# Performance work log

Hardware: AMD Instinct MI355X
Metric: run time of the kernel (lower is better)

Reference implementation:

```python
import jax, jax.numpy as jnp
import numpy as np

EMBED_DIM = 1024
N_HEADS = 16
HEAD_DIM = EMBED_DIM // N_HEADS
CHUNK = 64  # reward_data_gen_params['chunk_size']
B, T = 8, 1024


def setup_inputs() -> dict:
    key = jax.random.key(0)
    ks = jax.random.split(key, 9)
    s = 0.02
    return {
        "x": jax.random.normal(ks[0], (B, T, EMBED_DIM), dtype=jnp.float32),
        "Wq": jax.random.normal(ks[1], (EMBED_DIM, EMBED_DIM), dtype=jnp.float32) * s,
        "bq": jax.random.normal(ks[2], (EMBED_DIM,), dtype=jnp.float32) * s,
        "Wk": jax.random.normal(ks[3], (EMBED_DIM, EMBED_DIM), dtype=jnp.float32) * s,
        "bk": jax.random.normal(ks[4], (EMBED_DIM,), dtype=jnp.float32) * s,
        "Wv": jax.random.normal(ks[5], (EMBED_DIM, EMBED_DIM), dtype=jnp.float32) * s,
        "bv": jax.random.normal(ks[6], (EMBED_DIM,), dtype=jnp.float32) * s,
        "Wo": jax.random.normal(ks[7], (EMBED_DIM, EMBED_DIM), dtype=jnp.float32) * s,
        "bo": jax.random.normal(ks[8], (EMBED_DIM,), dtype=jnp.float32) * s,
        "attn_scale": jnp.full((1,), 1.0 / np.sqrt(HEAD_DIM), dtype=jnp.float32),
    }


def reference(x, Wq, bq, Wk, bk, Wv, bv, Wo, bo, attn_scale):
    Bsz, Tlen, C = x.shape
    H, D = N_HEADS, HEAD_DIM
    # torch Linear: y = x @ W.T + b
    q = (x @ Wq.T + bq).reshape(Bsz, Tlen, H, D).transpose(0, 2, 1, 3)  # [B,H,T,D]
    k = (x @ Wk.T + bk).reshape(Bsz, Tlen, H, D).transpose(0, 2, 1, 3)
    v = (x @ Wv.T + bv).reshape(Bsz, Tlen, H, D).transpose(0, 2, 1, 3)

    scores = jnp.einsum("bhqd,bhkd->bhqk", q, k) * attn_scale[0]  # [B,H,T,T]

    # Faithful reproduction of the chunked masking: the source only masks when
    # query-chunk >= key-chunk, which (given key>query implies key-chunk>=query-chunk)
    # reduces to masking key>query ONLY inside diagonal CHUNK x CHUNK blocks.
    idx = jnp.arange(Tlen)
    same_block = (idx[:, None] // CHUNK) == (idx[None, :] // CHUNK)
    mask = (idx[None, :] > idx[:, None]) & same_block  # [T,T] True => masked
    scores = jnp.where(mask[None, None], -jnp.inf, scores)

    w = jax.nn.softmax(scores, axis=-1)
    out = jnp.einsum("bhqk,bhkd->bhqd", w, v)  # [B,H,T,D]
    out = out.transpose(0, 2, 1, 3).reshape(Bsz, Tlen, C)
    return out @ Wo.T + bo
```

## Files before the change

### kernel.cpp

```cpp
#include <hip/hip_runtime.h>


typedef __bf16 bf16;
typedef __bf16 bf16x4 __attribute__((ext_vector_type(4)));
typedef __bf16 bf16x8 __attribute__((ext_vector_type(8)));
typedef float  f32x4  __attribute__((ext_vector_type(4)));

#define LOG2E 1.44269504088896340736f

__device__ __forceinline__ void async16(const bf16* g, bf16* l) {
  __builtin_amdgcn_global_load_lds(
      (const __attribute__((address_space(1))) void*)g,
      (__attribute__((address_space(3))) void*)l, 16, 0, 0);
}

#if __has_builtin(__builtin_amdgcn_exp2f)
#define EXP2F(x) __builtin_amdgcn_exp2f(x)
#else
#define EXP2F(x) exp2f(x)
#endif

__global__ __launch_bounds__(256) void k_convert(
    const float* __restrict__ x, const float* __restrict__ wq,
    const float* __restrict__ wk, const float* __restrict__ wv,
    const float* __restrict__ wo, bf16* __restrict__ xb, bf16* __restrict__ wb) {
  const int XV = (8192 * 1024) / 4;
  const int WV = (1024 * 1024) / 4;
  int i = blockIdx.x * 256 + threadIdx.x;
  const float4* src;
  bf16* dst;
  if (i < XV) {
    src = (const float4*)x + i;
    dst = xb + (size_t)i * 4;
  } else {
    int j = i - XV;
    int w = j >> 18;
    int r = j & (WV - 1);
    const float* s = (w == 0) ? wq : (w == 1) ? wk : (w == 2) ? wv : wo;
    src = (const float4*)s + r;
    dst = wb + (size_t)w * (1024 * 1024) + (size_t)r * 4;
  }
  float4 f = *src;
  bf16 tmp[4] = {(bf16)f.x, (bf16)f.y, (bf16)f.z, (bf16)f.w};
  *(uint2*)dst = *(uint2*)tmp;
}

__global__ __launch_bounds__(256) void k_gemm_qkv(
    const bf16* __restrict__ A, const bf16* __restrict__ W,
    const float* __restrict__ bq, const float* __restrict__ bk,
    const float* __restrict__ bv, const float* __restrict__ scale_p,
    bf16* __restrict__ qb, bf16* __restrict__ kb, bf16* __restrict__ vb) {
  __shared__ __attribute__((aligned(16))) bf16 As[8192];
  __shared__ __attribute__((aligned(16))) bf16 Bs[8192];
  const int tid = threadIdx.x, lane = tid & 63, wid = tid >> 6;
  const int quad = lane >> 4, l16 = lane & 15;
  const int wm = (wid & 1) * 64, wn = (wid >> 1) * 64;
  const int tileM = blockIdx.x * 128, tileN = blockIdx.y * 128;

  const int krow = lane >> 3;
  const int gc = (lane & 7) ^ krow;
  const bf16* Ap = A + (size_t)(tileM + wid * 8 + krow) * 1024 + gc * 8;
  const bf16* Bp = W + (size_t)(tileN + wid * 8 + krow) * 1024 + gc * 8;
  const int wofs = wid * 512;
  const int s7 = l16 & 7;

  f32x4 acc[4][4];
#pragma unroll
  for (int i = 0; i < 4; i++)
#pragma unroll
    for (int j = 0; j < 4; j++) acc[i][j] = (f32x4){0.f, 0.f, 0.f, 0.f};

  for (int it = 0; it < 16; it++) {
    const int k0 = it * 64;
#pragma unroll
    for (int rd = 0; rd < 4; rd++) {
      async16(Ap + (size_t)rd * 32768 + k0, &As[rd * 2048 + wofs]);
      async16(Bp + (size_t)rd * 32768 + k0, &Bs[rd * 2048 + wofs]);
    }
    __syncthreads();
#pragma unroll
    for (int kh = 0; kh < 2; kh++) {
      const int pc = ((kh * 4 + quad) ^ s7) * 8;
      bf16x8 af[4], bfr[4];
#pragma unroll
      for (int i = 0; i < 4; i++)
        af[i] = *(const bf16x8*)&As[(wm + i * 16 + l16) * 64 + pc];
#pragma unroll
      for (int j = 0; j < 4; j++)
        bfr[j] = *(const bf16x8*)&Bs[(wn + j * 16 + l16) * 64 + pc];
#pragma unroll
      for (int i = 0; i < 4; i++)
#pragma unroll
        for (int j = 0; j < 4; j++)
          acc[i][j] = __builtin_amdgcn_mfma_f32_16x16x32_bf16(af[i], bfr[j], acc[i][j], 0, 0, 0);
    }
    __syncthreads();
  }

  float qscale = scale_p[0] * LOG2E;
#pragma unroll
  for (int i = 0; i < 4; i++) {
    int m0 = tileM + wm + i * 16 + quad * 4;
    int b = m0 >> 10;
    int t0 = m0 & 1023;
#pragma unroll
    for (int j = 0; j < 4; j++) {
      int n = tileN + wn + j * 16 + l16;
      int which = n >> 10;
      int nm = n & 1023;
      int h = nm >> 6, d = nm & 63;
      float bias = ((which == 0) ? bq : (which == 1) ? bk : bv)[nm];
      if (which == 2) {
        bf16 tmp[4];
#pragma unroll
        for (int r = 0; r < 4; r++) tmp[r] = (bf16)(acc[i][j][r] + bias);
        size_t vidx = (((size_t)((b * 16 + h) * 64 + d)) << 10) | (size_t)t0;
        *(uint2*)&vb[vidx] = *(uint2*)tmp;
      } else {
#pragma unroll
        for (int r = 0; r < 4; r++) {
          float v = acc[i][j][r] + bias;
          size_t idx = (((size_t)(b * 16 + h) * 1024 + (t0 + r)) << 6) | (size_t)d;
          if (which == 0) qb[idx] = (bf16)(v * qscale);
          else            kb[idx] = (bf16)v;
        }
      }
    }
  }
}

__global__ __launch_bounds__(256) void k_gemm_out(
    const bf16* __restrict__ A, const bf16* __restrict__ W,
    const float* __restrict__ bo, float* __restrict__ out) {
  __shared__ __attribute__((aligned(16))) bf16 As[8192];
  __shared__ __attribute__((aligned(16))) bf16 Bs[8192];
  const int tid = threadIdx.x, lane = tid & 63, wid = tid >> 6;
  const int quad = lane >> 4, l16 = lane & 15;
  const int wm = (wid & 1) * 64, wn = (wid >> 1) * 64;
  const int tileM = blockIdx.x * 128, tileN = blockIdx.y * 128;

  const int krow = lane >> 3;
  const int gc = (lane & 7) ^ krow;
  const bf16* Ap = A + (size_t)(tileM + wid * 8 + krow) * 1024 + gc * 8;
  const bf16* Bp = W + (size_t)(tileN + wid * 8 + krow) * 1024 + gc * 8;
  const int wofs = wid * 512;
  const int s7 = l16 & 7;

  f32x4 acc[4][4];
#pragma unroll
  for (int i = 0; i < 4; i++)
#pragma unroll
    for (int j = 0; j < 4; j++) acc[i][j] = (f32x4){0.f, 0.f, 0.f, 0.f};

  for (int it = 0; it < 16; it++) {
    const int k0 = it * 64;
#pragma unroll
    for (int rd = 0; rd < 4; rd++) {
      async16(Ap + (size_t)rd * 32768 + k0, &As[rd * 2048 + wofs]);
      async16(Bp + (size_t)rd * 32768 + k0, &Bs[rd * 2048 + wofs]);
    }
    __syncthreads();
#pragma unroll
    for (int kh = 0; kh < 2; kh++) {
      const int pc = ((kh * 4 + quad) ^ s7) * 8;
      bf16x8 af[4], bfr[4];
#pragma unroll
      for (int i = 0; i < 4; i++)
        af[i] = *(const bf16x8*)&As[(wm + i * 16 + l16) * 64 + pc];
#pragma unroll
      for (int j = 0; j < 4; j++)
        bfr[j] = *(const bf16x8*)&Bs[(wn + j * 16 + l16) * 64 + pc];
#pragma unroll
      for (int i = 0; i < 4; i++)
#pragma unroll
        for (int j = 0; j < 4; j++)
          acc[i][j] = __builtin_amdgcn_mfma_f32_16x16x32_bf16(af[i], bfr[j], acc[i][j], 0, 0, 0);
    }
    __syncthreads();
  }

#pragma unroll
  for (int i = 0; i < 4; i++)
#pragma unroll
    for (int j = 0; j < 4; j++) {
      int n = tileN + wn + j * 16 + l16;
      float bias = bo[n];
#pragma unroll
      for (int r = 0; r < 4; r++) {
        int m = tileM + wm + i * 16 + quad * 4 + r;
        out[(size_t)m * 1024 + n] = acc[i][j][r] + bias;
      }
    }
}

__global__ __launch_bounds__(256, 2) void k_attn(
    const bf16* __restrict__ qb, const bf16* __restrict__ kb,
    const bf16* __restrict__ vb, bf16* __restrict__ attn) {
  __shared__ __attribute__((aligned(16))) bf16 KsF[2][4096];
  __shared__ __attribute__((aligned(16))) bf16 VsF[2][4096];
  const int tid = threadIdx.x, lane = tid & 63, wid = tid >> 6;
  const int quad = lane >> 4, l16 = lane & 15;
  const int bh = blockIdx.x;
  const int qt = blockIdx.y;
  const size_t base = (size_t)bh * (1024 * 64);
  const int qrow0 = qt * 256;

  bf16x8 qf[4][2];
#pragma unroll
  for (int s = 0; s < 4; s++) {
    const bf16* qrow = qb + base + (size_t)(qrow0 + s * 64 + wid * 16 + l16) * 64;
    qf[s][0] = *(const bf16x8*)(qrow + quad * 8);
    qf[s][1] = *(const bf16x8*)(qrow + 32 + quad * 8);
  }

  f32x4 oacc[4][4];
  float lpart[4];
#pragma unroll
  for (int s = 0; s < 4; s++) {
    lpart[s] = 0.f;
#pragma unroll
    for (int n = 0; n < 4; n++) oacc[s][n] = (f32x4){0.f, 0.f, 0.f, 0.f};
  }

  const int krow = lane >> 3;
  const int klc = (lane & 7) ^ krow;
  const bf16* kp = kb + base + (size_t)(wid * 8 + krow) * 64 + klc * 8;
  const bf16* vp = vb + base + (size_t)(wid * 8 + krow) * 1024 + klc * 8;
  const int wofs = wid * 512;

  async16(kp, &KsF[0][wofs]);
  async16(kp + 32 * 64, &KsF[0][2048 + wofs]);
  async16(vp, &VsF[0][wofs]);
  async16(vp + 32 * 1024, &VsF[0][2048 + wofs]);

  const int sw = l16 & 7;
  const int qpos16 = wid * 16 + l16;
  for (int kt = 0; kt < 16; kt++) {
    const int pp = kt & 1;
    __syncthreads();

    if (kt < 15) {
      const bf16* kpn = kp + (size_t)(kt + 1) * 4096;
      const bf16* vpn = vp + (size_t)(kt + 1) * 64;
      async16(kpn, &KsF[pp ^ 1][wofs]);
      async16(kpn + 32 * 64, &KsF[pp ^ 1][2048 + wofs]);
      async16(vpn, &VsF[pp ^ 1][wofs]);
      async16(vpn + 32 * 1024, &VsF[pp ^ 1][2048 + wofs]);
    }

    bf16x8 kf[4][2];
#pragma unroll
    for (int j = 0; j < 4; j++) {
      int row = (j * 16 + l16) * 64;
      kf[j][0] = *(const bf16x8*)&KsF[pp][row + ((quad ^ sw) * 8)];
      kf[j][1] = *(const bf16x8*)&KsF[pp][row + (((quad + 4) ^ sw) * 8)];
    }
    bf16x8 pfrag[4][2];
#pragma unroll
    for (int s = 0; s < 4; s++) {
      f32x4 sv[4];
#pragma unroll
      for (int j = 0; j < 4; j++) {
        f32x4 z = (f32x4){0.f, 0.f, 0.f, 0.f};
        z = __builtin_amdgcn_mfma_f32_16x16x32_bf16(kf[j][0], qf[s][0], z, 0, 0, 0);
        z = __builtin_amdgcn_mfma_f32_16x16x32_bf16(kf[j][1], qf[s][1], z, 0, 0, 0);
        sv[j] = z;
      }
      if (qt * 4 + s == kt) {
#pragma unroll
        for (int j = 0; j < 4; j++) {
          int kbase = j * 16 + quad * 4;
#pragma unroll
          for (int r = 0; r < 4; r++)
            if (kbase + r > qpos16) sv[j][r] = -1e30f;
        }
      }
#pragma unroll
      for (int t = 0; t < 2; t++) {
        union { bf16x8 v; bf16 e[8]; } pu;
#pragma unroll
        for (int j2 = 0; j2 < 2; j2++)
#pragma unroll
          for (int r = 0; r < 4; r++) {
            float p = EXP2F(sv[t * 2 + j2][r]);
            lpart[s] += p;
            pu.e[j2 * 4 + r] = (bf16)p;
          }
        pfrag[s][t] = pu.v;
      }
    }

#pragma unroll
    for (int t = 0; t < 2; t++) {
      bf16x8 vf[4];
#pragma unroll
      for (int n = 0; n < 4; n++) {
        int rb = (n * 16 + l16) * 64;
        int g1 = 4 * t + (quad >> 1);
        int off = (quad & 1) * 4;
        union { bf16x8 v; bf16x4 h[2]; } u;
        u.h[0] = *(const bf16x4*)&VsF[pp][rb + ((g1 ^ sw) * 8) + off];
        u.h[1] = *(const bf16x4*)&VsF[pp][rb + (((g1 + 2) ^ sw) * 8) + off];
        vf[n] = u.v;
      }
#pragma unroll
      for (int s = 0; s < 4; s++)
#pragma unroll
        for (int n = 0; n < 4; n++)
          oacc[s][n] = __builtin_amdgcn_mfma_f32_16x16x32_bf16(vf[n], pfrag[s][t], oacc[s][n], 0, 0, 0);
    }
  }

  const int b = bh >> 4, h = bh & 15;
#pragma unroll
  for (int s = 0; s < 4; s++) {
    float l = lpart[s];
    l += __shfl_xor(l, 16, 64);
    l += __shfl_xor(l, 32, 64);
    float inv = 1.0f / l;
    int t = qrow0 + s * 64 + wid * 16 + l16;
    size_t rowb = ((size_t)(b * 1024 + t) << 10) + h * 64 + quad * 4;
#pragma unroll
    for (int n = 0; n < 4; n++) {
      bf16 tmp[4];
#pragma unroll
      for (int r = 0; r < 4; r++) tmp[r] = (bf16)(oacc[s][n][r] * inv);
      *(uint2*)&attn[rowb + n * 16] = *(uint2*)tmp;
    }
  }
}

extern "C" void kernel_launch(void* const* d_in, const int* in_sizes, int n_in,
                              void* d_out, int out_size, void* d_ws, size_t ws_size,
                              hipStream_t stream) {
  const float* x     = (const float*)d_in[0];
  const float* Wq    = (const float*)d_in[1];
  const float* bq    = (const float*)d_in[2];
  const float* Wk    = (const float*)d_in[3];
  const float* bk    = (const float*)d_in[4];
  const float* Wv    = (const float*)d_in[5];
  const float* bv    = (const float*)d_in[6];
  const float* Wo    = (const float*)d_in[7];
  const float* bo    = (const float*)d_in[8];
  const float* scale = (const float*)d_in[9];

  char* ws = (char*)d_ws;
  bf16* xb   = (bf16*)(ws);
  bf16* wb   = (bf16*)(ws + (size_t)(16 << 20));
  bf16* qb   = (bf16*)(ws + (size_t)(24 << 20));
  bf16* kb   = (bf16*)(ws + (size_t)(40 << 20));
  bf16* vb   = (bf16*)(ws + (size_t)(56 << 20));
  bf16* attn = xb;
  float* out = (float*)d_out;

  hipLaunchKernelGGL(k_convert, dim3(12288), dim3(256), 0, stream,
                     x, Wq, Wk, Wv, Wo, xb, wb);
  hipLaunchKernelGGL(k_gemm_qkv, dim3(64, 24), dim3(256), 0, stream,
                     xb, wb, bq, bk, bv, scale, qb, kb, vb);
  hipLaunchKernelGGL(k_attn, dim3(128, 4), dim3(256), 0, stream,
                     qb, kb, vb, attn);
  hipLaunchKernelGGL(k_gemm_out, dim3(64, 8), dim3(256), 0, stream,
                     attn, wb + (size_t)3072 * 1024, bo, out);
}
```

Baseline: 231.3 us.

## Double-buffer GEMM LDS tiles and unroll attention K/V ping-pong by two

Both the QKV and output projection GEMMs switch from a single LDS buffer (load, barrier, compute, barrier) to two ping-pong buffers. The async global-to-LDS copy of the next K slab is issued before computing the current one, so memory latency is meant to hide behind MFMA work. The attention loop keeps its existing double buffering but is unrolled by two with lambdas, so the buffer addresses are compile-time constants rather than indexed by parity. The cost is twice the LDS per GEMM block, which may lower occupancy, plus larger code.

```diff
diff --git a/kernel.cpp b/kernel.cpp
--- a/kernel.cpp
+++ b/kernel.cpp
@@ -50,8 +50,8 @@
     const float* __restrict__ bq, const float* __restrict__ bk,
     const float* __restrict__ bv, const float* __restrict__ scale_p,
     bf16* __restrict__ qb, bf16* __restrict__ kb, bf16* __restrict__ vb) {
-  __shared__ __attribute__((aligned(16))) bf16 As[8192];
-  __shared__ __attribute__((aligned(16))) bf16 Bs[8192];
+  __shared__ __attribute__((aligned(16))) bf16 As0[8192], As1[8192];
+  __shared__ __attribute__((aligned(16))) bf16 Bs0[8192], Bs1[8192];
   const int tid = threadIdx.x, lane = tid & 63, wid = tid >> 6;
   const int quad = lane >> 4, l16 = lane & 15;
   const int wm = (wid & 1) * 64, wn = (wid >> 1) * 64;
@@ -70,31 +70,42 @@
 #pragma unroll
     for (int j = 0; j < 4; j++) acc[i][j] = (f32x4){0.f, 0.f, 0.f, 0.f};
 
-  for (int it = 0; it < 16; it++) {
-    const int k0 = it * 64;
+  auto stage = [&](int slab, bf16* Ad, bf16* Bd) {
+    const size_t k0 = (size_t)slab * 64;
 #pragma unroll
     for (int rd = 0; rd < 4; rd++) {
-      async16(Ap + (size_t)rd * 32768 + k0, &As[rd * 2048 + wofs]);
-      async16(Bp + (size_t)rd * 32768 + k0, &Bs[rd * 2048 + wofs]);
-    }
-    __syncthreads();
+      async16(Ap + (size_t)rd * 32768 + k0, Ad + rd * 2048 + wofs);
+      async16(Bp + (size_t)rd * 32768 + k0, Bd + rd * 2048 + wofs);
+    }
+  };
+  auto compute = [&](const bf16* Ab, const bf16* Bb) {
 #pragma unroll
     for (int kh = 0; kh < 2; kh++) {
       const int pc = ((kh * 4 + quad) ^ s7) * 8;
       bf16x8 af[4], bfr[4];
 #pragma unroll
       for (int i = 0; i < 4; i++)
-        af[i] = *(const bf16x8*)&As[(wm + i * 16 + l16) * 64 + pc];
+        af[i] = *(const bf16x8*)&Ab[(wm + i * 16 + l16) * 64 + pc];
 #pragma unroll
       for (int j = 0; j < 4; j++)
-        bfr[j] = *(const bf16x8*)&Bs[(wn + j * 16 + l16) * 64 + pc];
+        bfr[j] = *(const bf16x8*)&Bb[(wn + j * 16 + l16) * 64 + pc];
 #pragma unroll
       for (int i = 0; i < 4; i++)
 #pragma unroll
         for (int j = 0; j < 4; j++)
           acc[i][j] = __builtin_amdgcn_mfma_f32_16x16x32_bf16(af[i], bfr[j], acc[i][j], 0, 0, 0);
     }
-    __syncthreads();
+  };
+
+  stage(0, As0, Bs0);
+#pragma unroll 1
+  for (int it2 = 0; it2 < 8; it2++) {
+    __syncthreads();
+    stage(2 * it2 + 1, As1, Bs1);
+    compute(As0, Bs0);
+    __syncthreads();
+    if (it2 < 7) stage(2 * it2 + 2, As0, Bs0);
+    compute(As1, Bs1);
   }
 
   float qscale = scale_p[0] * LOG2E;
@@ -132,8 +143,8 @@
 __global__ __launch_bounds__(256) void k_gemm_out(
     const bf16* __restrict__ A, const bf16* __restrict__ W,
     const float* __restrict__ bo, float* __restrict__ out) {
-  __shared__ __attribute__((aligned(16))) bf16 As[8192];
-  __shared__ __attribute__((aligned(16))) bf16 Bs[8192];
+  __shared__ __attribute__((aligned(16))) bf16 As0[8192], As1[8192];
+  __shared__ __attribute__((aligned(16))) bf16 Bs0[8192], Bs1[8192];
   const int tid = threadIdx.x, lane = tid & 63, wid = tid >> 6;
   const int quad = lane >> 4, l16 = lane & 15;
   const int wm = (wid & 1) * 64, wn = (wid >> 1) * 64;
@@ -152,31 +163,42 @@
 #pragma unroll
     for (int j = 0; j < 4; j++) acc[i][j] = (f32x4){0.f, 0.f, 0.f, 0.f};
 
-  for (int it = 0; it < 16; it++) {
-    const int k0 = it * 64;
+  auto stage = [&](int slab, bf16* Ad, bf16* Bd) {
+    const size_t k0 = (size_t)slab * 64;
 #pragma unroll
     for (int rd = 0; rd < 4; rd++) {
-      async16(Ap + (size_t)rd * 32768 + k0, &As[rd * 2048 + wofs]);
-      async16(Bp + (size_t)rd * 32768 + k0, &Bs[rd * 2048 + wofs]);
-    }
-    __syncthreads();
+      async16(Ap + (size_t)rd * 32768 + k0, Ad + rd * 2048 + wofs);
+      async16(Bp + (size_t)rd * 32768 + k0, Bd + rd * 2048 + wofs);
+    }
+  };
+  auto compute = [&](const bf16* Ab, const bf16* Bb) {
 #pragma unroll
     for (int kh = 0; kh < 2; kh++) {
       const int pc = ((kh * 4 + quad) ^ s7) * 8;
       bf16x8 af[4], bfr[4];
 #pragma unroll
       for (int i = 0; i < 4; i++)
-        af[i] = *(const bf16x8*)&As[(wm + i * 16 + l16) * 64 + pc];
+        af[i] = *(const bf16x8*)&Ab[(wm + i * 16 + l16) * 64 + pc];
 #pragma unroll
       for (int j = 0; j < 4; j++)
-        bfr[j] = *(const bf16x8*)&Bs[(wn + j * 16 + l16) * 64 + pc];
+        bfr[j] = *(const bf16x8*)&Bb[(wn + j * 16 + l16) * 64 + pc];
 #pragma unroll
       for (int i = 0; i < 4; i++)
 #pragma unroll
         for (int j = 0; j < 4; j++)
           acc[i][j] = __builtin_amdgcn_mfma_f32_16x16x32_bf16(af[i], bfr[j], acc[i][j], 0, 0, 0);
     }
-    __syncthreads();
+  };
+
+  stage(0, As0, Bs0);
+#pragma unroll 1
+  for (int it2 = 0; it2 < 8; it2++) {
+    __syncthreads();
+    stage(2 * it2 + 1, As1, Bs1);
+    compute(As0, Bs0);
+    __syncthreads();
+    if (it2 < 7) stage(2 * it2 + 2, As0, Bs0);
+    compute(As1, Bs1);
   }
 
 #pragma unroll
@@ -196,8 +218,8 @@
 __global__ __launch_bounds__(256, 2) void k_attn(
     const bf16* __restrict__ qb, const bf16* __restrict__ kb,
     const bf16* __restrict__ vb, bf16* __restrict__ attn) {
-  __shared__ __attribute__((aligned(16))) bf16 KsF[2][4096];
-  __shared__ __attribute__((aligned(16))) bf16 VsF[2][4096];
+  __shared__ __attribute__((aligned(16))) bf16 Ks0[4096], Ks1[4096];
+  __shared__ __attribute__((aligned(16))) bf16 Vs0[4096], Vs1[4096];
   const int tid = threadIdx.x, lane = tid & 63, wid = tid >> 6;
   const int quad = lane >> 4, l16 = lane & 15;
   const int bh = blockIdx.x;
@@ -228,32 +250,25 @@
   const bf16* vp = vb + base + (size_t)(wid * 8 + krow) * 1024 + klc * 8;
   const int wofs = wid * 512;
 
-  async16(kp, &KsF[0][wofs]);
-  async16(kp + 32 * 64, &KsF[0][2048 + wofs]);
-  async16(vp, &VsF[0][wofs]);
-  async16(vp + 32 * 1024, &VsF[0][2048 + wofs]);
+  auto stage_kv = [&](int kt, bf16* Kd, bf16* Vd) {
+    const bf16* kpn = kp + (size_t)kt * 4096;
+    const bf16* vpn = vp + (size_t)kt * 64;
+    async16(kpn, Kd + wofs);
+    async16(kpn + 32 * 64, Kd + 2048 + wofs);
+    async16(vpn, Vd + wofs);
+    async16(vpn + 32 * 1024, Vd + 2048 + wofs);
+  };
 
   const int sw = l16 & 7;
   const int qpos16 = wid * 16 + l16;
-  for (int kt = 0; kt < 16; kt++) {
-    const int pp = kt & 1;
-    __syncthreads();
-
-    if (kt < 15) {
-      const bf16* kpn = kp + (size_t)(kt + 1) * 4096;
-      const bf16* vpn = vp + (size_t)(kt + 1) * 64;
-      async16(kpn, &KsF[pp ^ 1][wofs]);
-      async16(kpn + 32 * 64, &KsF[pp ^ 1][2048 + wofs]);
-      async16(vpn, &VsF[pp ^ 1][wofs]);
-      async16(vpn + 32 * 1024, &VsF[pp ^ 1][2048 + wofs]);
-    }
-
+
+  auto body = [&](int kt, const bf16* Kb, const bf16* Vb) {
     bf16x8 kf[4][2];
 #pragma unroll
     for (int j = 0; j < 4; j++) {
       int row = (j * 16 + l16) * 64;
-      kf[j][0] = *(const bf16x8*)&KsF[pp][row + ((quad ^ sw) * 8)];
-      kf[j][1] = *(const bf16x8*)&KsF[pp][row + (((quad + 4) ^ sw) * 8)];
+      kf[j][0] = *(const bf16x8*)&Kb[row + ((quad ^ sw) * 8)];
+      kf[j][1] = *(const bf16x8*)&Kb[row + (((quad + 4) ^ sw) * 8)];
     }
     bf16x8 pfrag[4][2];
 #pragma unroll
@@ -299,8 +314,8 @@
         int g1 = 4 * t + (quad >> 1);
         int off = (quad & 1) * 4;
         union { bf16x8 v; bf16x4 h[2]; } u;
-        u.h[0] = *(const bf16x4*)&VsF[pp][rb + ((g1 ^ sw) * 8) + off];
-        u.h[1] = *(const bf16x4*)&VsF[pp][rb + (((g1 + 2) ^ sw) * 8) + off];
+        u.h[0] = *(const bf16x4*)&Vb[rb + ((g1 ^ sw) * 8) + off];
+        u.h[1] = *(const bf16x4*)&Vb[rb + (((g1 + 2) ^ sw) * 8) + off];
         vf[n] = u.v;
       }
 #pragma unroll
@@ -309,6 +324,17 @@
         for (int n = 0; n < 4; n++)
           oacc[s][n] = __builtin_amdgcn_mfma_f32_16x16x32_bf16(vf[n], pfrag[s][t], oacc[s][n], 0, 0, 0);
     }
+  };
+
+  stage_kv(0, Ks0, Vs0);
+#pragma unroll 1
+  for (int kt2 = 0; kt2 < 8; kt2++) {
+    __syncthreads();
+    stage_kv(2 * kt2 + 1, Ks1, Vs1);
+    body(2 * kt2, Ks0, Vs0);
+    __syncthreads();
+    if (kt2 < 7) stage_kv(2 * kt2 + 2, Ks0, Vs0);
+    body(2 * kt2 + 1, Ks1, Vs1);
   }
 
   const int b = bh >> 4, h = bh & 15;
```

Result: slower. 239.8 us (+3.7%).
